# Kernel tuning notes

Hardware: AMD Instinct MI355X
Metric: run time of the kernel (lower is better)

Reference implementation:

```python
import jax, jax.numpy as jnp
import numpy as np

N = 50000
E = 800000
D = 128
H = 8
DH = D // H


def setup_inputs() -> dict:
    key = jax.random.key(0)
    ks = jax.random.split(key, 8)
    x = jax.random.normal(ks[0], (N, D), dtype=jnp.float32)
    src = jax.random.randint(ks[1], (E,), 0, N, dtype=jnp.int32)
    dst = jax.random.randint(ks[2], (E,), 0, N, dtype=jnp.int32)
    s = 1.0 / np.sqrt(D)
    w_qkv = jax.random.uniform(ks[3], (3 * D, D), jnp.float32, -s, s)
    b_qkv = jax.random.uniform(ks[4], (3 * D,), jnp.float32, -s, s)
    w_out = jax.random.uniform(ks[5], (D, D), jnp.float32, -s, s)
    b_out = jax.random.uniform(ks[6], (D,), jnp.float32, -s, s)
    return {"x": x, "src": src, "dst": dst, "w_qkv": w_qkv, "b_qkv": b_qkv,
            "w_out": w_out, "b_out": b_out}


def reference(x, src, dst, w_qkv, b_qkv, w_out, b_out):
    n = x.shape[0]
    coef = 1.0 / np.sqrt(DH)
    qkv = (x @ w_qkv.T + b_qkv).reshape(n, H, 3 * DH)
    q, k, v = qkv[..., :DH], qkv[..., DH:2 * DH], qkv[..., 2 * DH:]
    # per-edge scores: dot(k[src], q[dst]) per head -> [E, H]
    scores = jnp.einsum('ehd,ehd->eh', k[src], q[dst]) * coef
    # edge softmax over edges sharing the same destination node
    smax = jax.ops.segment_max(scores, dst, num_segments=n)  # [N, H]
    smax = jnp.where(jnp.isfinite(smax), smax, 0.0)
    ex = jnp.exp(scores - smax[dst])                          # [E, H]
    denom = jax.ops.segment_sum(ex, dst, num_segments=n)      # [N, H]
    probs = ex / jnp.maximum(denom[dst], 1e-30)
    # weighted aggregation of source values -> [N, H, DH]
    agg = jax.ops.segment_sum(probs[:, :, None] * v[src], dst, num_segments=n)
    out = agg.reshape(n, D) @ w_out.T + b_out
    return out
```

## Files before the change

kernel.cpp:

```cpp
#include <hip/hip_runtime.h>
#include <math.h>

#define DD   128
#define NQKV 384
#define CAP  128

typedef __attribute__((ext_vector_type(8))) short          bf16x8;
typedef __attribute__((ext_vector_type(8))) unsigned short ushort8;
typedef __attribute__((ext_vector_type(4))) float          f32x4;
typedef __attribute__((ext_vector_type(2))) float          f32x2;

__device__ __forceinline__ unsigned short f2bf(float f) {
    unsigned u = __float_as_uint(f);
    u += 0x7fffu + ((u >> 16) & 1u);
    return (unsigned short)(u >> 16);
}
__device__ __forceinline__ float bf2f(unsigned short h) {
    return __uint_as_float(((unsigned)h) << 16);
}
__device__ __forceinline__ float bflo(unsigned u) { return __uint_as_float(u << 16); }
__device__ __forceinline__ float bfhi(unsigned u) { return __uint_as_float(u & 0xffff0000u); }
__device__ __forceinline__ f32x2 unpk(unsigned u) {
    f32x2 r; r.x = bflo(u); r.y = bfhi(u); return r;
}

__global__ void scatter_fixed_kernel(const int* __restrict__ src, const int* __restrict__ dst,
                                     int* __restrict__ counts, int* __restrict__ lists, int E) {
    int t = blockIdx.x * blockDim.x + threadIdx.x;
    int base = t * 8;
    if (base >= E) return;
    if (base + 8 <= E) {
        int4 d0 = *(const int4*)(dst + base);
        int4 d1 = *(const int4*)(dst + base + 4);
        int4 s0 = *(const int4*)(src + base);
        int4 s1 = *(const int4*)(src + base + 4);
        int dd[8] = {d0.x, d0.y, d0.z, d0.w, d1.x, d1.y, d1.z, d1.w};
        int ss[8] = {s0.x, s0.y, s0.z, s0.w, s1.x, s1.y, s1.z, s1.w};
        int pos[8];
        #pragma unroll
        for (int i = 0; i < 8; ++i) pos[i] = atomicAdd(&counts[dd[i]], 1);
        #pragma unroll
        for (int i = 0; i < 8; ++i)
            if (pos[i] < CAP) lists[(size_t)dd[i] * CAP + pos[i]] = ss[i];
    } else {
        for (int e = base; e < E; ++e) {
            int d = dst[e];
            int pos = atomicAdd(&counts[d], 1);
            if (pos < CAP) lists[(size_t)d * CAP + pos] = src[e];
        }
    }
}

#define TM 128
#define TN 128
#define LDA 40

__global__ __launch_bounds__(256, 3) void qkv_gemm_kernel(
    const float* __restrict__ X, const float* __restrict__ W,
    const float* __restrict__ bias, unsigned short* __restrict__ Cq,
    unsigned short* __restrict__ Ck, unsigned short* __restrict__ Cv, int M)
{
    __shared__ unsigned short As[TM * LDA];
    __shared__ unsigned short Bs_h[TN * LDA];
    __shared__ unsigned short Bs_l[TN * LDA];

    const int tid  = threadIdx.x;
    const int l    = tid & 63;
    const int wv   = tid >> 6;
    const int quad = l >> 4;
    const int l15  = l & 15;
    const int wm   = (wv & 1) * 64;
    const int wn   = (wv >> 1) * 64;
    const int n0   = blockIdx.x * TN;
    const int m0   = blockIdx.y * TM;

    f32x4 acc[4][4];
    #pragma unroll
    for (int i = 0; i < 4; ++i)
        #pragma unroll
        for (int j = 0; j < 4; ++j) acc[i][j] = (f32x4)0.f;

    #pragma unroll
    for (int kc = 0; kc < DD; kc += 32) {
        #pragma unroll
        for (int it = 0; it < 2; ++it) {
            int idx = tid + it * 256;
            int row = idx >> 2;
            int pc  = idx & 3;
            int loff = row * LDA + pc * 8;
            ushort8 va = 0;
            if (m0 + row < M) {
                const float4* xp = (const float4*)(X + (size_t)(m0 + row) * DD + kc + pc * 8);
                float4 a0 = xp[0], a1 = xp[1];
                float v[8] = {a0.x,a0.y,a0.z,a0.w,a1.x,a1.y,a1.z,a1.w};
                #pragma unroll
                for (int t = 0; t < 8; ++t) va[t] = f2bf(v[t]);
            }
            *(ushort8*)&As[loff] = va;
            const float4* wp = (const float4*)(W + (size_t)(n0 + row) * DD + kc + pc * 8);
            float4 b0 = wp[0], b1 = wp[1];
            float wvv[8] = {b0.x,b0.y,b0.z,b0.w,b1.x,b1.y,b1.z,b1.w};
            ushort8 vh, vl;
            #pragma unroll
            for (int t = 0; t < 8; ++t) {
                unsigned short hh = f2bf(wvv[t]);
                vh[t] = hh;
                vl[t] = f2bf(wvv[t] - bf2f(hh));
            }
            *(ushort8*)&Bs_h[loff] = vh;
            *(ushort8*)&Bs_l[loff] = vl;
        }
        __syncthreads();

        bf16x8 ah[4], bh[4], bl[4];
        #pragma unroll
        for (int mt = 0; mt < 4; ++mt)
            ah[mt] = *(const bf16x8*)&As[(wm + mt * 16 + l15) * LDA + quad * 8];
        #pragma unroll
        for (int nt = 0; nt < 4; ++nt) {
            int off = (wn + nt * 16 + l15) * LDA + quad * 8;
            bh[nt] = *(const bf16x8*)&Bs_h[off];
            bl[nt] = *(const bf16x8*)&Bs_l[off];
        }
        #pragma unroll
        for (int mt = 0; mt < 4; ++mt)
            #pragma unroll
            for (int nt = 0; nt < 4; ++nt) {
                acc[mt][nt] = __builtin_amdgcn_mfma_f32_16x16x32_bf16(ah[mt], bh[nt], acc[mt][nt], 0, 0, 0);
                acc[mt][nt] = __builtin_amdgcn_mfma_f32_16x16x32_bf16(ah[mt], bl[nt], acc[mt][nt], 0, 0, 0);
            }
        __syncthreads();
    }

    #pragma unroll
    for (int nt = 0; nt < 4; ++nt) {
        int j = n0 + wn + nt * 16 + l15;
        float bj = bias[j];
        int h = j / 48;
        int r = j - h * 48;
        int seg = (r >= 32) ? 2 : ((r >= 16) ? 1 : 0);
        int bc  = h * 16 + r - seg * 16;
        unsigned short* dstp = (seg == 0 ? Cq : (seg == 1 ? Ck : Cv));
        #pragma unroll
        for (int mt = 0; mt < 4; ++mt)
            #pragma unroll
            for (int rr = 0; rr < 4; ++rr) {
                int m = m0 + wm + mt * 16 + quad * 4 + rr;
                if (m < M) dstp[(size_t)m * DD + bc] = f2bf(acc[mt][nt][rr] + bj);
            }
    }
}

__global__ __launch_bounds__(256, 3) void out_gemm_kernel(
    const unsigned short* __restrict__ A, const float* __restrict__ W,
    const float* __restrict__ bias, float* __restrict__ C, int M)
{
    __shared__ unsigned short As[TM * LDA];
    __shared__ unsigned short Bs_h[TN * LDA];
    __shared__ unsigned short Bs_l[TN * LDA];

    const int tid  = threadIdx.x;
    const int l    = tid & 63;
    const int wv   = tid >> 6;
    const int quad = l >> 4;
    const int l15  = l & 15;
    const int wm   = (wv & 1) * 64;
    const int wn   = (wv >> 1) * 64;
    const int m0   = blockIdx.x * TM;

    f32x4 acc[4][4];
    #pragma unroll
    for (int i = 0; i < 4; ++i)
        #pragma unroll
        for (int j = 0; j < 4; ++j) acc[i][j] = (f32x4)0.f;

    #pragma unroll
    for (int kc = 0; kc < DD; kc += 32) {
        #pragma unroll
        for (int it = 0; it < 2; ++it) {
            int idx = tid + it * 256;
            int row = idx >> 2;
            int pc  = idx & 3;
            int loff = row * LDA + pc * 8;
            ushort8 va = 0;
            if (m0 + row < M)
                va = *(const ushort8*)(A + (size_t)(m0 + row) * DD + kc + pc * 8);
            *(ushort8*)&As[loff] = va;
            const float4* wp = (const float4*)(W + (size_t)row * DD + kc + pc * 8);
            float4 b0 = wp[0], b1 = wp[1];
            float wvv[8] = {b0.x,b0.y,b0.z,b0.w,b1.x,b1.y,b1.z,b1.w};
            ushort8 vh, vl;
            #pragma unroll
            for (int t = 0; t < 8; ++t) {
                unsigned short hh = f2bf(wvv[t]);
                vh[t] = hh;
                vl[t] = f2bf(wvv[t] - bf2f(hh));
            }
            *(ushort8*)&Bs_h[loff] = vh;
            *(ushort8*)&Bs_l[loff] = vl;
        }
        __syncthreads();

        bf16x8 ah[4], bh[4], bl[4];
        #pragma unroll
        for (int mt = 0; mt < 4; ++mt)
            ah[mt] = *(const bf16x8*)&As[(wm + mt * 16 + l15) * LDA + quad * 8];
        #pragma unroll
        for (int nt = 0; nt < 4; ++nt) {
            int off = (wn + nt * 16 + l15) * LDA + quad * 8;
            bh[nt] = *(const bf16x8*)&Bs_h[off];
            bl[nt] = *(const bf16x8*)&Bs_l[off];
        }
        #pragma unroll
        for (int mt = 0; mt < 4; ++mt)
            #pragma unroll
            for (int nt = 0; nt < 4; ++nt) {
                acc[mt][nt] = __builtin_amdgcn_mfma_f32_16x16x32_bf16(ah[mt], bh[nt], acc[mt][nt], 0, 0, 0);
                acc[mt][nt] = __builtin_amdgcn_mfma_f32_16x16x32_bf16(ah[mt], bl[nt], acc[mt][nt], 0, 0, 0);
            }
        __syncthreads();
    }

    #pragma unroll
    for (int nt = 0; nt < 4; ++nt) {
        int j = wn + nt * 16 + l15;
        float bj = bias[j];
        #pragma unroll
        for (int mt = 0; mt < 4; ++mt)
            #pragma unroll
            for (int rr = 0; rr < 4; ++rr) {
                int m = m0 + wm + mt * 16 + quad * 4 + rr;
                if (m < M) C[(size_t)m * DD + j] = acc[mt][nt][rr] + bj;
            }
    }
}

__global__ __launch_bounds__(256) void wave_attn_kernel(
    const unsigned short* __restrict__ qbf, const unsigned short* __restrict__ kbf,
    const unsigned short* __restrict__ vbf, const int* __restrict__ lists,
    const int* __restrict__ counts,
    unsigned short* __restrict__ agg, int N)
{
    const int lane = threadIdx.x & 63;
    const int n = blockIdx.x * 4 + (threadIdx.x >> 6);
    if (n >= N) return;

    const int h = lane >> 3;
    const int e = lane & 7;

    const int deg = min(counts[n], CAP);
    const size_t obase = (size_t)n * DD + 2 * lane;
    if (deg == 0) {
        *(unsigned*)(agg + obase) = 0u;
        return;
    }

    const int row0 = n * CAP;

    const uint4* qp = (const uint4*)(qbf + (size_t)n * DD + h * 16);
    const uint4 qa = qp[0], qb = qp[1];
    const f32x2 qv[8] = { unpk(qa.x), unpk(qa.y), unpk(qa.z), unpk(qa.w),
                          unpk(qb.x), unpk(qb.y), unpk(qb.z), unpk(qb.w) };

    int cur = lists[row0 + min(e, deg - 1)];
    int nxt = lists[row0 + min(8 + e, deg - 1)];

    const uint4* kp0 = (const uint4*)(kbf + (size_t)cur * DD + h * 16);
    uint4 ka = kp0[0], kb = kp0[1];
    unsigned vv[8];
    #pragma unroll
    for (int ee = 0; ee < 8; ++ee)
        vv[ee] = *(const unsigned*)(vbf + (size_t)__shfl(cur, ee) * DD + 2 * lane);

    float l_run = 0.f;
    f32x2 acc2 = (f32x2)0.f;

    for (int c = 0; c < deg; c += 8) {
        const int cnt = min(8, deg - c);
        const bool more = (c + 8 < deg);

        const int nn = lists[row0 + min(c + 16 + e, deg - 1)];

        uint4 k1a = ka, k1b = kb;
        unsigned vn[8];
        #pragma unroll
        for (int ee = 0; ee < 8; ++ee) vn[ee] = vv[ee];
        if (more) {
            const uint4* kp = (const uint4*)(kbf + (size_t)nxt * DD + h * 16);
            k1a = kp[0]; k1b = kp[1];
            #pragma unroll
            for (int ee = 0; ee < 8; ++ee)
                vn[ee] = *(const unsigned*)(vbf + (size_t)__shfl(nxt, ee) * DD + 2 * lane);
        }

        f32x2 d = unpk(ka.x) * qv[0];
        d = unpk(ka.y) * qv[1] + d;
        d = unpk(ka.z) * qv[2] + d;
        d = unpk(ka.w) * qv[3] + d;
        d = unpk(kb.x) * qv[4] + d;
        d = unpk(kb.y) * qv[5] + d;
        d = unpk(kb.z) * qv[6] + d;
        d = unpk(kb.w) * qv[7] + d;
        const float s = d.x + d.y;

        const float p = (e < cnt) ? __expf(s * 0.25f) : 0.f;
        l_run += p;

        #pragma unroll
        for (int ee = 0; ee < 8; ++ee) {
            const float pe = __shfl(p, (lane & 0x38) | ee);
            acc2 = unpk(vv[ee]) * pe + acc2;
        }

        ka = k1a; kb = k1b;
        #pragma unroll
        for (int ee = 0; ee < 8; ++ee) vv[ee] = vn[ee];
        cur = nxt; nxt = nn;
    }

    l_run += __shfl_xor(l_run, 1);
    l_run += __shfl_xor(l_run, 2);
    l_run += __shfl_xor(l_run, 4);

    const float inv = 1.f / fmaxf(l_run, 1e-30f);
    const float o0 = acc2.x * inv, o1 = acc2.y * inv;
    *(unsigned*)(agg + obase) = (unsigned)f2bf(o0) | ((unsigned)f2bf(o1) << 16);
}

extern "C" void kernel_launch(void* const* d_in, const int* in_sizes, int n_in,
                              void* d_out, int out_size, void* d_ws, size_t ws_size,
                              hipStream_t stream) {
    const float* x     = (const float*)d_in[0];
    const int*   src   = (const int*)  d_in[1];
    const int*   dst   = (const int*)  d_in[2];
    const float* w_qkv = (const float*)d_in[3];
    const float* b_qkv = (const float*)d_in[4];
    const float* w_out = (const float*)d_in[5];
    const float* b_out = (const float*)d_in[6];
    float* out = (float*)d_out;

    const int N = in_sizes[0] / DD;
    const int E = in_sizes[1];

    typedef unsigned short u16;
    char* ws = (char*)d_ws;
    u16* qbf   = (u16*)ws;   ws += (size_t)N * DD * sizeof(u16);
    u16* kbf   = (u16*)ws;   ws += (size_t)N * DD * sizeof(u16);
    u16* vbf   = (u16*)ws;   ws += (size_t)N * DD * sizeof(u16);
    u16* aggb  = (u16*)ws;   ws += (size_t)N * DD * sizeof(u16);
    int* counts = (int*)ws;  ws += (size_t)N * sizeof(int);
    int* lists  = (int*)ws;  ws += (size_t)N * CAP * sizeof(int);

    const int nsb = ((E + 7) / 8 + 255) / 256;
    const int MB  = (N + TM - 1) / TM;

    hipMemsetAsync(counts, 0, (size_t)N * sizeof(int), stream);

    scatter_fixed_kernel<<<nsb, 256, 0, stream>>>(src, dst, counts, lists, E);

    qkv_gemm_kernel<<<dim3(NQKV / TN, MB), 256, 0, stream>>>(
        x, w_qkv, b_qkv, qbf, kbf, vbf, N);

    wave_attn_kernel<<<(N + 3) / 4, 256, 0, stream>>>(
        qbf, kbf, vbf, lists, counts, aggb, N);

    out_gemm_kernel<<<MB, 256, 0, stream>>>(
        aggb, w_out, b_out, out, N);
}
```

Measured before the change: 240.5 us.

## Fuse all stages into one persistent cooperative kernel with grid syncs

Replaces the memset, scatter, QKV GEMM, attention and output GEMM launches with a single cooperative persistent kernel. Stages are separated by grid-wide syncs, and the scatter jobs run in the same phase as the QKV GEMM tiles so they overlap. The aim is to remove launch gaps and tail idle time between kernels. In exchange, the attention phase loses the occupancy it had as a standalone kernel: it is limited by the GEMM's shared memory and launch bounds and runs as a grid-stride loop, and the grid syncs add their own cost.

Result: slower. 616.3 us (+156.3%).

```diff
diff --git a/kernel.cpp b/kernel.cpp
--- a/kernel.cpp
+++ b/kernel.cpp
@@ -1,14 +1,21 @@
 #include <hip/hip_runtime.h>
+#include <hip/hip_cooperative_groups.h>
 #include <math.h>
+
+namespace cg = cooperative_groups;
 
 #define DD   128
 #define NQKV 384
 #define CAP  128
+#define TM   128
+#define TN   128
+#define LDA  40
 
 typedef __attribute__((ext_vector_type(8))) short          bf16x8;
 typedef __attribute__((ext_vector_type(8))) unsigned short ushort8;
 typedef __attribute__((ext_vector_type(4))) float          f32x4;
 typedef __attribute__((ext_vector_type(2))) float          f32x2;
+typedef unsigned short u16;
 
 __device__ __forceinline__ unsigned short f2bf(float f) {
     unsigned u = __float_as_uint(f);
@@ -24,10 +31,11 @@
     f32x2 r; r.x = bflo(u); r.y = bfhi(u); return r;
 }
 
-__global__ void scatter_fixed_kernel(const int* __restrict__ src, const int* __restrict__ dst,
-                                     int* __restrict__ counts, int* __restrict__ lists, int E) {
-    int t = blockIdx.x * blockDim.x + threadIdx.x;
-    int base = t * 8;
+__device__ __forceinline__ void scatter_job(int j, const int* __restrict__ src,
+                                            const int* __restrict__ dst,
+                                            int* __restrict__ counts,
+                                            int* __restrict__ lists, int E) {
+    int base = (j * 256 + (int)threadIdx.x) * 8;
     if (base >= E) return;
     if (base + 8 <= E) {
         int4 d0 = *(const int4*)(dst + base);
@@ -51,19 +59,12 @@
     }
 }
 
-#define TM 128
-#define TN 128
-#define LDA 40
-
-__global__ __launch_bounds__(256, 3) void qkv_gemm_kernel(
-    const float* __restrict__ X, const float* __restrict__ W,
-    const float* __restrict__ bias, unsigned short* __restrict__ Cq,
-    unsigned short* __restrict__ Ck, unsigned short* __restrict__ Cv, int M)
+__device__ __forceinline__ void qkv_tile(
+    int m0, int n0, const float* __restrict__ X, const float* __restrict__ W,
+    const float* __restrict__ bias, u16* __restrict__ Cq, u16* __restrict__ Ck,
+    u16* __restrict__ Cv, int M,
+    unsigned short* As, unsigned short* Bs_h, unsigned short* Bs_l)
 {
-    __shared__ unsigned short As[TM * LDA];
-    __shared__ unsigned short Bs_h[TN * LDA];
-    __shared__ unsigned short Bs_l[TN * LDA];
-
     const int tid  = threadIdx.x;
     const int l    = tid & 63;
     const int wv   = tid >> 6;
@@ -71,8 +72,6 @@
     const int l15  = l & 15;
     const int wm   = (wv & 1) * 64;
     const int wn   = (wv >> 1) * 64;
-    const int n0   = blockIdx.x * TN;
-    const int m0   = blockIdx.y * TM;
 
     f32x4 acc[4][4];
     #pragma unroll
@@ -140,7 +139,7 @@
         int r = j - h * 48;
         int seg = (r >= 32) ? 2 : ((r >= 16) ? 1 : 0);
         int bc  = h * 16 + r - seg * 16;
-        unsigned short* dstp = (seg == 0 ? Cq : (seg == 1 ? Ck : Cv));
+        u16* dstp = (seg == 0 ? Cq : (seg == 1 ? Ck : Cv));
         #pragma unroll
         for (int mt = 0; mt < 4; ++mt)
             #pragma unroll
@@ -151,14 +150,11 @@
     }
 }
 
-__global__ __launch_bounds__(256, 3) void out_gemm_kernel(
-    const unsigned short* __restrict__ A, const float* __restrict__ W,
-    const float* __restrict__ bias, float* __restrict__ C, int M)
+__device__ __forceinline__ void out_tile(
+    int m0, const u16* __restrict__ A, const float* __restrict__ W,
+    const float* __restrict__ bias, float* __restrict__ C, int M,
+    unsigned short* As, unsigned short* Bs_h, unsigned short* Bs_l)
 {
-    __shared__ unsigned short As[TM * LDA];
-    __shared__ unsigned short Bs_h[TN * LDA];
-    __shared__ unsigned short Bs_l[TN * LDA];
-
     const int tid  = threadIdx.x;
     const int l    = tid & 63;
     const int wv   = tid >> 6;
@@ -166,7 +162,6 @@
     const int l15  = l & 15;
     const int wm   = (wv & 1) * 64;
     const int wn   = (wv >> 1) * 64;
-    const int m0   = blockIdx.x * TM;
 
     f32x4 acc[4][4];
     #pragma unroll
@@ -235,14 +230,12 @@
     }
 }
 
-__global__ __launch_bounds__(256) void wave_attn_kernel(
-    const unsigned short* __restrict__ qbf, const unsigned short* __restrict__ kbf,
-    const unsigned short* __restrict__ vbf, const int* __restrict__ lists,
-    const int* __restrict__ counts,
-    unsigned short* __restrict__ agg, int N)
+__device__ __forceinline__ void attn_node(
+    int n, const u16* __restrict__ qbf, const u16* __restrict__ kbf,
+    const u16* __restrict__ vbf, const int* __restrict__ lists,
+    const int* __restrict__ counts, u16* __restrict__ agg, int N)
 {
     const int lane = threadIdx.x & 63;
-    const int n = blockIdx.x * 4 + (threadIdx.x >> 6);
     if (n >= N) return;
 
     const int h = lane >> 3;
@@ -256,7 +249,6 @@
     }
 
     const int row0 = n * CAP;
-
     const uint4* qp = (const uint4*)(qbf + (size_t)n * DD + h * 16);
     const uint4 qa = qp[0], qb = qp[1];
     const f32x2 qv[8] = { unpk(qa.x), unpk(qa.y), unpk(qa.z), unpk(qa.w),
@@ -323,8 +315,54 @@
     l_run += __shfl_xor(l_run, 4);
 
     const float inv = 1.f / fmaxf(l_run, 1e-30f);
-    const float o0 = acc2.x * inv, o1 = acc2.y * inv;
-    *(unsigned*)(agg + obase) = (unsigned)f2bf(o0) | ((unsigned)f2bf(o1) << 16);
+    *(unsigned*)(agg + obase) = (unsigned)f2bf(acc2.x * inv) |
+                                ((unsigned)f2bf(acc2.y * inv) << 16);
+}
+
+__global__ __launch_bounds__(256, 4) void mega_kernel(
+    const float* __restrict__ x, const int* __restrict__ esrc,
+    const int* __restrict__ edst, const float* __restrict__ w_qkv,
+    const float* __restrict__ b_qkv, const float* __restrict__ w_out,
+    const float* __restrict__ b_out, float* __restrict__ out,
+    u16* __restrict__ qbf, u16* __restrict__ kbf, u16* __restrict__ vbf,
+    u16* __restrict__ aggb, int* __restrict__ counts, int* __restrict__ lists,
+    int N, int E)
+{
+    cg::grid_group grid = cg::this_grid();
+
+    __shared__ unsigned short As[TM * LDA];
+    __shared__ unsigned short Bs_h[TN * LDA];
+    __shared__ unsigned short Bs_l[TN * LDA];
+
+    const int G     = gridDim.x;
+    const int MB    = (N + TM - 1) / TM;
+    const int NSCAT = (E + 2047) / 2048;
+    const int QKV_T = 3 * MB;
+    const int NB_AT = (N + 3) / 4;
+
+    for (int i = blockIdx.x * 256 + threadIdx.x; i < N; i += G * 256)
+        counts[i] = 0;
+    grid.sync();
+
+    for (int j = blockIdx.x; j < NSCAT + QKV_T; j += G) {
+        if (j < NSCAT) {
+            scatter_job(j, esrc, edst, counts, lists, E);
+        } else {
+            int t = j - NSCAT;
+            qkv_tile((t / 3) * TM, (t % 3) * TN, x, w_qkv, b_qkv,
+                     qbf, kbf, vbf, N, As, Bs_h, Bs_l);
+        }
+    }
+    __threadfence();
+    grid.sync();
+
+    for (int vb = blockIdx.x; vb < NB_AT; vb += G)
+        attn_node(vb * 4 + (threadIdx.x >> 6), qbf, kbf, vbf, lists, counts, aggb, N);
+    __threadfence();
+    grid.sync();
+
+    for (int j = blockIdx.x; j < MB; j += G)
+        out_tile(j * TM, aggb, w_out, b_out, out, N, As, Bs_h, Bs_l);
 }
 
 extern "C" void kernel_launch(void* const* d_in, const int* in_sizes, int n_in,
@@ -339,10 +377,9 @@
     const float* b_out = (const float*)d_in[6];
     float* out = (float*)d_out;
 
-    const int N = in_sizes[0] / DD;
-    const int E = in_sizes[1];
-
-    typedef unsigned short u16;
+    int N = in_sizes[0] / DD;
+    int E = in_sizes[1];
+
     char* ws = (char*)d_ws;
     u16* qbf   = (u16*)ws;   ws += (size_t)N * DD * sizeof(u16);
     u16* kbf   = (u16*)ws;   ws += (size_t)N * DD * sizeof(u16);
@@ -351,19 +388,17 @@
     int* counts = (int*)ws;  ws += (size_t)N * sizeof(int);
     int* lists  = (int*)ws;  ws += (size_t)N * CAP * sizeof(int);
 
-    const int nsb = ((E + 7) / 8 + 255) / 256;
-    const int MB  = (N + TM - 1) / TM;
-
-    hipMemsetAsync(counts, 0, (size_t)N * sizeof(int), stream);
-
-    scatter_fixed_kernel<<<nsb, 256, 0, stream>>>(src, dst, counts, lists, E);
-
-    qkv_gemm_kernel<<<dim3(NQKV / TN, MB), 256, 0, stream>>>(
-        x, w_qkv, b_qkv, qbf, kbf, vbf, N);
-
-    wave_attn_kernel<<<(N + 3) / 4, 256, 0, stream>>>(
-        qbf, kbf, vbf, lists, counts, aggb, N);
-
-    out_gemm_kernel<<<MB, 256, 0, stream>>>(
-        aggb, w_out, b_out, out, N);
-}
+    int bpc = 0;
+    hipOccupancyMaxActiveBlocksPerMultiprocessor(&bpc, (const void*)mega_kernel, 256, 0);
+    if (bpc < 1) bpc = 1;
+    if (bpc > 4) bpc = 4;
+    int grid = bpc * 256;
+
+    void* args[] = { (void*)&x, (void*)&src, (void*)&dst, (void*)&w_qkv,
+                     (void*)&b_qkv, (void*)&w_out, (void*)&b_out, (void*)&out,
+                     (void*)&qbf, (void*)&kbf, (void*)&vbf, (void*)&aggb,
+                     (void*)&counts, (void*)&lists, (void*)&N, (void*)&E };
+
+    hipLaunchCooperativeKernel((const void*)mega_kernel, dim3(grid), dim3(256),
+                               args, 0, stream);
+}
```
